# Optimization experiments

Hardware: AMD Instinct MI355X
Metric: run time of the kernel (lower is better)

Reference implementation:

```python
import jax, jax.numpy as jnp
import numpy as np

B, S = 4, 2048
O, I, G = 11008, 4096, 128
NG = I // G  # 32 groups

def setup_inputs() -> dict:
    key = jax.random.key(0)
    k1, k2, k3, k4, k5 = jax.random.split(key, 5)
    x = jax.random.normal(k1, (B, S, I), dtype=jnp.float32)
    # packed 4-bit weights: each int holds two nibbles (low, high)
    qweight = jax.random.randint(k2, (O, I // 2), 0, 256, dtype=jnp.int32)
    scale = jax.random.uniform(k3, (O, NG, 1), dtype=jnp.float32) * 0.01
    zero_point = jax.random.uniform(k4, (O, NG, 1), dtype=jnp.float32) * 15.0
    bias = jax.random.normal(k5, (O,), dtype=jnp.float32) * 0.01
    return {"x": x, "qweight": qweight, "scale": scale, "zero_point": zero_point, "bias": bias}

def _dequantize_4bit(qweight, scale, zero_point):
    low = qweight & 15          # [O, I//2]
    high = (qweight >> 4) & 15  # [O, I//2]
    # interleave low/high nibbles along the last dim -> [O, I]
    unpacked = jnp.stack((low, high), axis=-1).reshape(O, I).astype(jnp.float32)
    # group-wise affine dequant
    w = ((unpacked.reshape(O, NG, G) - zero_point) * scale).reshape(O, I)
    return w

def reference(x, qweight, scale, zero_point, bias):
    w = _dequantize_4bit(qweight, scale, zero_point)  # [O, I]
    # F.linear: x @ w.T + bias
    return jnp.einsum('bsi,oi->bso', x, w) + bias
```

## Files before the change

### kernel.cpp

```cpp
#include <hip/hip_runtime.h>
#include <cstdint>

static constexpr int Mdim = 8192;
static constexpr int Ndim = 11008;
static constexpr int Kdim = 4096;
static constexpr int NGRP = 32;

#define BM 128
#define BN 128
#define BK 64

typedef __bf16 bf16x8 __attribute__((ext_vector_type(8)));
typedef float floatx4 __attribute__((ext_vector_type(4)));
typedef unsigned short ushort8_t __attribute__((ext_vector_type(8)));

__device__ __forceinline__ unsigned short f2bf(float f) {
  union { float f; uint32_t u; } v; v.f = f;
  uint32_t u = v.u;
  return (unsigned short)((u + 0x7fffu + ((u >> 16) & 1u)) >> 16);
}

__device__ __forceinline__ void gload16(const void* g, void* l) {
  __builtin_amdgcn_global_load_lds(
      (const __attribute__((address_space(1))) void*)g,
      (__attribute__((address_space(3))) void*)l, 16, 0, 0);
}

__global__ __launch_bounds__(256) void cast_x_kernel(const float* __restrict__ x,
                                                     unsigned short* __restrict__ xb) {
  int i = blockIdx.x * 256 + threadIdx.x;
  float4 f = ((const float4*)x)[i];
  ushort4 o;
  o.x = f2bf(f.x); o.y = f2bf(f.y); o.z = f2bf(f.z); o.w = f2bf(f.w);
  ((ushort4*)xb)[i] = o;
}

__global__ __launch_bounds__(256) void dequant_w_kernel(const int* __restrict__ qw,
                                                        const float* __restrict__ scale,
                                                        const float* __restrict__ zp,
                                                        unsigned short* __restrict__ wb) {
  int idx = blockIdx.x * 256 + threadIdx.x;
  int o  = idx >> 9;
  int j4 = idx & 511;
  int g  = j4 >> 4;
  float s = scale[o * NGRP + g];
  float z = zp[o * NGRP + g];
  int4 q = ((const int4*)qw)[idx];
  int qs[4] = {q.x, q.y, q.z, q.w};
  ushort8_t r;
#pragma unroll
  for (int t = 0; t < 4; ++t) {
    float lo = (float)(qs[t] & 15);
    float hi = (float)((qs[t] >> 4) & 15);
    r[2 * t]     = f2bf((lo - z) * s);
    r[2 * t + 1] = f2bf((hi - z) * s);
  }
  *(ushort8_t*)(wb + (size_t)o * Kdim + (size_t)j4 * 8) = r;
}

__global__ __launch_bounds__(256, 2) void gemm_kernel(const unsigned short* __restrict__ Xb,
                                                      const unsigned short* __restrict__ Wb,
                                                      const float* __restrict__ bias,
                                                      float* __restrict__ out) {
  __shared__ unsigned short As[BM * BK];
  __shared__ unsigned short Bs[BN * BK];

  const int tid  = threadIdx.x;
  const int wave = tid >> 6;
  const int lane = tid & 63;
  const int wm   = wave & 1;
  const int wn   = wave >> 1;

  const int row0 = blockIdx.x * BM;
  const int col0 = blockIdx.y * BN;

  const int srow = wave * 32 + (lane >> 3);
  const int sw   = (lane >> 3) & 7;
  const int scol = (((lane & 7) ^ sw) << 3);

  const unsigned short* ag = Xb + (size_t)(row0 + srow) * Kdim + scol;
  const unsigned short* bg = Wb + (size_t)(col0 + srow) * Kdim + scol;
  unsigned short* al = &As[(wave * 32) * BK];
  unsigned short* bl = &Bs[(wave * 32) * BK];

  floatx4 acc[4][4];
#pragma unroll
  for (int i = 0; i < 4; ++i)
#pragma unroll
    for (int j = 0; j < 4; ++j) acc[i][j] = (floatx4){0.f, 0.f, 0.f, 0.f};

  for (int k0 = 0; k0 < Kdim; k0 += BK) {
#pragma unroll
    for (int i = 0; i < 4; ++i) {
      gload16(ag + (size_t)(i * 8) * Kdim, al + i * 8 * BK);
      gload16(bg + (size_t)(i * 8) * Kdim, bl + i * 8 * BK);
    }
    ag += BK; bg += BK;
    __syncthreads();

#pragma unroll
    for (int kk = 0; kk < BK; kk += 32) {
      bf16x8 af[4], bfr[4];
#pragma unroll
      for (int t = 0; t < 4; ++t) {
        const int co = ((((kk >> 3) + (lane >> 4)) ^ (lane & 7)) << 3);
        af[t]  = *(const bf16x8*)&As[(wm * 64 + t * 16 + (lane & 15)) * BK + co];
        bfr[t] = *(const bf16x8*)&Bs[(wn * 64 + t * 16 + (lane & 15)) * BK + co];
      }
#pragma unroll
      for (int tm = 0; tm < 4; ++tm)
#pragma unroll
        for (int tn = 0; tn < 4; ++tn)
          acc[tm][tn] = __builtin_amdgcn_mfma_f32_16x16x32_bf16(af[tm], bfr[tn], acc[tm][tn], 0, 0, 0);
    }
    __syncthreads();
  }

  const int m_base = row0 + wm * 64;
  const int n_base = col0 + wn * 64;
#pragma unroll
  for (int tn = 0; tn < 4; ++tn) {
    const int n = n_base + tn * 16 + (lane & 15);
    const float bv = bias[n];
#pragma unroll
    for (int tm = 0; tm < 4; ++tm) {
      const int m0 = m_base + tm * 16 + (lane >> 4) * 4;
#pragma unroll
      for (int r = 0; r < 4; ++r)
        out[(size_t)(m0 + r) * Ndim + n] = acc[tm][tn][r] + bv;
    }
  }
}

extern "C" void kernel_launch(void* const* d_in, const int* in_sizes, int n_in,
                              void* d_out, int out_size, void* d_ws, size_t ws_size,
                              hipStream_t stream) {
  const float* x     = (const float*)d_in[0];
  const int*   qw    = (const int*)d_in[1];
  const float* scale = (const float*)d_in[2];
  const float* zp    = (const float*)d_in[3];
  const float* bias  = (const float*)d_in[4];
  float* out = (float*)d_out;

  unsigned short* xb = (unsigned short*)d_ws;
  unsigned short* wb = xb + (size_t)Mdim * Kdim;

  cast_x_kernel<<<(Mdim * Kdim / 4) / 256, 256, 0, stream>>>(x, xb);
  dequant_w_kernel<<<(Ndim * 512) / 256, 256, 0, stream>>>(qw, scale, zp, wb);
  gemm_kernel<<<dim3(Mdim / BM, Ndim / BN), 256, 0, stream>>>(xb, wb, bias, out);
}
```

Measured before the change: 1.219 ms.

## Restructure GEMM into 256x256 tiles with double-buffered LDS and XCD-aware block remap

The GEMM now uses 512-thread blocks computing 256x256 tiles, with a 2-stage double-buffered LDS pipeline that uses global_load_lds and explicit vmcnt waits. A block-id remap spreads consecutive tiles across the 8 XCDs, s_setprio raises priority around the MFMA clusters, and output stores are nontemporal. The aim is to overlap global loads with MFMA work, raise arithmetic intensity, and improve L2 locality. The trade-offs are more register pressure from the 8x4 accumulators per wave and 128KB of LDS per block, which limits occupancy.

After: 1.167 ms. 4.3% less time.

```diff
diff --git a/kernel.cpp b/kernel.cpp
--- a/kernel.cpp
+++ b/kernel.cpp
@@ -6,9 +6,12 @@
 static constexpr int Kdim = 4096;
 static constexpr int NGRP = 32;
 
-#define BM 128
-#define BN 128
+#define BM 256
+#define BN 256
 #define BK 64
+#define NT (Kdim / BK)
+#define NBLK ((Mdim / BM) * (Ndim / BN))
+#define CPX (NBLK / 8)
 
 typedef __bf16 bf16x8 __attribute__((ext_vector_type(8)));
 typedef float floatx4 __attribute__((ext_vector_type(4)));
@@ -58,76 +61,105 @@
   *(ushort8_t*)(wb + (size_t)o * Kdim + (size_t)j4 * 8) = r;
 }
 
-__global__ __launch_bounds__(256, 2) void gemm_kernel(const unsigned short* __restrict__ Xb,
+__global__ __launch_bounds__(512, 2) void gemm_kernel(const unsigned short* __restrict__ Xb,
                                                       const unsigned short* __restrict__ Wb,
                                                       const float* __restrict__ bias,
                                                       float* __restrict__ out) {
-  __shared__ unsigned short As[BM * BK];
-  __shared__ unsigned short Bs[BN * BK];
+  __shared__ unsigned short lds[2 * 512 * BK];
 
   const int tid  = threadIdx.x;
   const int wave = tid >> 6;
   const int lane = tid & 63;
-  const int wm   = wave & 1;
-  const int wn   = wave >> 1;
+  const int wm   = wave >> 2;
+  const int wn   = wave & 3;
 
-  const int row0 = blockIdx.x * BM;
-  const int col0 = blockIdx.y * BN;
+  const int bid  = blockIdx.x;
+  const int wg   = (bid & 7) * CPX + (bid >> 3);
+  const int mb   = wg & 31;
+  const int nb   = wg >> 5;
+  const int row0 = mb * BM;
+  const int col0 = nb * BN;
 
-  const int srow = wave * 32 + (lane >> 3);
-  const int sw   = (lane >> 3) & 7;
-  const int scol = (((lane & 7) ^ sw) << 3);
+  const unsigned short* gp[8];
+#pragma unroll
+  for (int j = 0; j < 8; ++j) {
+    const int q   = j * 512 + tid;
+    const int row = q >> 3;
+    const int cg  = (q & 7) ^ (row & 7);
+    gp[j] = (row < 256)
+          ? Xb + (size_t)(row0 + row) * Kdim + cg * 8
+          : Wb + (size_t)(col0 + row - 256) * Kdim + cg * 8;
+  }
+  const int ldsoff = wave * 64 * 8;
 
-  const unsigned short* ag = Xb + (size_t)(row0 + srow) * Kdim + scol;
-  const unsigned short* bg = Wb + (size_t)(col0 + srow) * Kdim + scol;
-  unsigned short* al = &As[(wave * 32) * BK];
-  unsigned short* bl = &Bs[(wave * 32) * BK];
+#define STAGE(Lb) do { _Pragma("unroll")                                  \
+  for (int j = 0; j < 8; ++j) {                                           \
+    gload16(gp[j], (Lb) + ldsoff + j * 512 * 8);                          \
+    gp[j] += BK;                                                          \
+  } } while (0)
 
-  floatx4 acc[4][4];
+  floatx4 acc[8][4];
 #pragma unroll
-  for (int i = 0; i < 4; ++i)
+  for (int i = 0; i < 8; ++i)
 #pragma unroll
     for (int j = 0; j < 4; ++j) acc[i][j] = (floatx4){0.f, 0.f, 0.f, 0.f};
 
-  for (int k0 = 0; k0 < Kdim; k0 += BK) {
+  auto phase = [&](const unsigned short* L, int kk) {
+    bf16x8 af[8], bf[4];
+    const int co = ((((kk >> 3) + (lane >> 4)) ^ (lane & 7)) << 3);
+    const int rA = wm * 128 + (lane & 15);
+    const int rB = 256 + wn * 64 + (lane & 15);
 #pragma unroll
-    for (int i = 0; i < 4; ++i) {
-      gload16(ag + (size_t)(i * 8) * Kdim, al + i * 8 * BK);
-      gload16(bg + (size_t)(i * 8) * Kdim, bl + i * 8 * BK);
+    for (int m = 0; m < 8; ++m) af[m] = *(const bf16x8*)&L[(rA + m * 16) * BK + co];
+#pragma unroll
+    for (int n = 0; n < 4; ++n) bf[n] = *(const bf16x8*)&L[(rB + n * 16) * BK + co];
+    __builtin_amdgcn_s_setprio(1);
+#pragma unroll
+    for (int m = 0; m < 8; ++m)
+#pragma unroll
+      for (int n = 0; n < 4; ++n)
+        acc[m][n] = __builtin_amdgcn_mfma_f32_16x16x32_bf16(af[m], bf[n], acc[m][n], 0, 0, 0);
+    __builtin_amdgcn_s_setprio(0);
+  };
+
+  STAGE(lds);
+  STAGE(lds + 512 * BK);
+  asm volatile("s_waitcnt vmcnt(8)" ::: "memory");
+  __builtin_amdgcn_s_barrier();
+  __builtin_amdgcn_sched_barrier(0);
+
+  for (int t = 0; t < NT; ++t) {
+    unsigned short* L = (unsigned short*)lds + (t & 1) * (512 * BK);
+
+    phase(L, 0);
+    __builtin_amdgcn_s_barrier();
+    phase(L, 32);
+
+    if (t < NT - 2) {
+      asm volatile("" ::: "memory");
+      __builtin_amdgcn_s_barrier();
+      STAGE(L);
+      asm volatile("s_waitcnt vmcnt(8)" ::: "memory");
+      __builtin_amdgcn_s_barrier();
+      __builtin_amdgcn_sched_barrier(0);
+    } else if (t == NT - 2) {
+      asm volatile("s_waitcnt vmcnt(0)" ::: "memory");
+      __builtin_amdgcn_s_barrier();
+      __builtin_amdgcn_sched_barrier(0);
     }
-    ag += BK; bg += BK;
-    __syncthreads();
+  }
+#undef STAGE
 
 #pragma unroll
-    for (int kk = 0; kk < BK; kk += 32) {
-      bf16x8 af[4], bfr[4];
+  for (int n = 0; n < 4; ++n) {
+    const int nn = col0 + wn * 64 + n * 16 + (lane & 15);
+    const float bv = bias[nn];
 #pragma unroll
-      for (int t = 0; t < 4; ++t) {
-        const int co = ((((kk >> 3) + (lane >> 4)) ^ (lane & 7)) << 3);
-        af[t]  = *(const bf16x8*)&As[(wm * 64 + t * 16 + (lane & 15)) * BK + co];
-        bfr[t] = *(const bf16x8*)&Bs[(wn * 64 + t * 16 + (lane & 15)) * BK + co];
-      }
-#pragma unroll
-      for (int tm = 0; tm < 4; ++tm)
-#pragma unroll
-        for (int tn = 0; tn < 4; ++tn)
-          acc[tm][tn] = __builtin_amdgcn_mfma_f32_16x16x32_bf16(af[tm], bfr[tn], acc[tm][tn], 0, 0, 0);
-    }
-    __syncthreads();
-  }
-
-  const int m_base = row0 + wm * 64;
-  const int n_base = col0 + wn * 64;
-#pragma unroll
-  for (int tn = 0; tn < 4; ++tn) {
-    const int n = n_base + tn * 16 + (lane & 15);
-    const float bv = bias[n];
-#pragma unroll
-    for (int tm = 0; tm < 4; ++tm) {
-      const int m0 = m_base + tm * 16 + (lane >> 4) * 4;
+    for (int m = 0; m < 8; ++m) {
+      const int m0 = row0 + wm * 128 + m * 16 + (lane >> 4) * 4;
 #pragma unroll
       for (int r = 0; r < 4; ++r)
-        out[(size_t)(m0 + r) * Ndim + n] = acc[tm][tn][r] + bv;
+        __builtin_nontemporal_store(acc[m][n][r] + bv, &out[(size_t)(m0 + r) * Ndim + nn]);
     }
   }
 }
@@ -147,5 +179,5 @@
 
   cast_x_kernel<<<(Mdim * Kdim / 4) / 256, 256, 0, stream>>>(x, xb);
   dequant_w_kernel<<<(Ndim * 512) / 256, 256, 0, stream>>>(qw, scale, zp, wb);
-  gemm_kernel<<<dim3(Mdim / BM, Ndim / BN), 256, 0, stream>>>(xb, wb, bias, out);
+  gemm_kernel<<<NBLK, 512, 0, stream>>>(xb, wb, bias, out);
 }
```
